# Performance work log

Hardware: AMD Instinct MI355X
Metric: run time of the kernel (lower is better)

Reference implementation:

```python
import math
import jax, jax.numpy as jnp
import numpy as np

B = 8          # number of graphs in the batch
NMAX = 256     # max nodes per graph (padding size)
K = 128        # num_kernels
H = 32         # num_heads
NTYPE = 101    # max_node_type + 1


def setup_inputs() -> dict:
    key = jax.random.key(0)
    ks = jax.random.split(key, 10)
    sizes = np.asarray(NMAX - np.arange(B) * 16, dtype=np.int32)  # 256,240,...,144 -> ragged
    N = int(sizes.sum())  # 1600
    coord = jax.random.normal(ks[0], (N, 3), dtype=jnp.float32) * 3.0
    node_type = jax.random.randint(ks[1], (N,), 0, NTYPE, dtype=jnp.int32)
    gaussian_means = jax.random.uniform(ks[2], (1, K), minval=0.0, maxval=3.0, dtype=jnp.float32)
    gaussian_stds = jax.random.uniform(ks[3], (1, K), minval=0.0, maxval=3.0, dtype=jnp.float32)
    # nn.Embedding(max_node_type+1, 2) tables; original init is const(0)/const(1),
    # we perturb so the computation is non-degenerate.
    mul_w = jax.random.normal(ks[4], (NTYPE, 2), dtype=jnp.float32) * 0.1
    bias_w = 1.0 + jax.random.normal(ks[5], (NTYPE, 2), dtype=jnp.float32) * 0.1
    W1 = jax.random.normal(ks[6], (K, K), dtype=jnp.float32) / math.sqrt(K)
    b1 = jnp.zeros((K,), dtype=jnp.float32)
    W2 = jax.random.normal(ks[7], (K, H), dtype=jnp.float32) / math.sqrt(K)
    b2 = jnp.zeros((H,), dtype=jnp.float32)
    return {
        "coord": coord,
        "gaussian_means": gaussian_means,
        "gaussian_stds": gaussian_stds,
        "mul_w": mul_w,
        "bias_w": bias_w,
        "W1": W1,
        "b1": b1,
        "W2": W2,
        "b2": b2,
        "node_type": node_type,
        "batch_num_nodes": jnp.asarray(sizes),
    }


def reference(coord, gaussian_means, gaussian_stds, mul_w, bias_w, W1, b1, W2, b2,
              node_type, batch_num_nodes):
    N = coord.shape[0]
    offsets = jnp.concatenate([jnp.zeros((1,), dtype=batch_num_nodes.dtype),
                               jnp.cumsum(batch_num_nodes)[:-1]])
    ar = jnp.arange(NMAX)
    idx = offsets[:, None] + ar[None, :]                     # [B, n] flat node index per graph slot
    valid = ar[None, :] < batch_num_nodes[:, None]           # [B, n] node mask
    idx_c = jnp.clip(idx, 0, N - 1)
    pc = coord[idx_c]                                        # [B, n, 3] padded coords
    pt = node_type[idx_c]                                    # [B, n]

    # pairwise Euclidean distance (torch.cdist p=2), sqrt-safe at 0
    diff = pc[:, :, None, :] - pc[:, None, :, :]             # [B, n, n, 3]
    sq = jnp.sum(diff * diff, axis=-1)                       # [B, n, n]
    nz = sq > 0
    dist = jnp.where(nz, jnp.sqrt(jnp.where(nz, sq, 1.0)), 0.0)

    # outer-sum of per-node (src, dst) scaling embeddings
    mul_e = mul_w[pt]                                        # [B, n, 2]
    bias_e = bias_w[pt]
    mul = mul_e[:, :, None, 0] + mul_e[:, None, :, 1]        # [B, n, n]
    bias = bias_e[:, :, None, 0] + bias_e[:, None, :, 1]
    scaled = mul * dist + bias                               # [B, n, n]

    means = gaussian_means.reshape(-1)                       # [K]
    stds = jnp.abs(gaussian_stds.reshape(-1)) + 0.01         # [K]
    z = (scaled[..., None] - means) / stds                   # [B, n, n, K]
    gk = jnp.exp(-0.5 * z * z) / (-math.sqrt(2.0 * math.pi) * stds)

    h = jax.nn.gelu(gk @ W1 + b1, approximate=False)         # exact gelu like torch F.gelu
    out = h @ W2 + b2                                        # [B, n, n, H]

    pair = valid[:, :, None] & valid[:, None, :]             # padded positions -> -inf
    return jnp.where(pair[..., None], out, -jnp.inf)
```

## Files before the change

### kernel.cpp

```cpp
#include <hip/hip_runtime.h>
#include <math.h>

#define NMAXC 256
#define KC 128
#define HC 32
#define BC 8
#define TP 128
#define NEG_SENTINEL (-1.0e30f)
#define LOG2E 1.4426950408889634f

typedef __bf16 bf16x8 __attribute__((ext_vector_type(8)));
typedef float  f32x16 __attribute__((ext_vector_type(16)));
union FragU { uint4 u; bf16x8 v; };

#define EXP2F(x) __builtin_amdgcn_exp2f(x)

__device__ __forceinline__ unsigned pack2(float lo, float hi) {
    return __builtin_amdgcn_perm(__float_as_uint(hi), __float_as_uint(lo), 0x07060302u);
}

__global__ __launch_bounds__(256) void se3d_prep(const float* __restrict__ W1,
                                                 const float* __restrict__ W2,
                                                 const float* __restrict__ gm,
                                                 const float* __restrict__ gs,
                                                 unsigned* __restrict__ wsu) {
    int t = blockIdx.x * 256 + threadIdx.x;
    if (t < 2048) {
        int f = t >> 6, l = t & 63;
        int mt = f >> 3, ks = f & 7;
        int c  = mt * 32 + (l & 31);
        int k0 = ks * 16 + 8 * (l >> 5);
        unsigned u[4];
#pragma unroll
        for (int p = 0; p < 4; ++p)
            u[p] = pack2(-W1[(k0 + 2 * p) * KC + c], -W1[(k0 + 2 * p + 1) * KC + c]);
        ((uint4*)wsu)[t] = make_uint4(u[0], u[1], u[2], u[3]);
    } else if (t < 2560) {
        int x = t - 2048;
        int ft = x >> 6, l = x & 63;
        int hi = l >> 5, ln = l & 31;
        unsigned u[4];
#pragma unroll
        for (int d = 0; d < 4; ++d) {
            int c0 = 32 * (ft >> 1) + 16 * (ft & 1) + 8 * (d >> 1) + 4 * hi + 2 * (d & 1);
            u[d] = pack2(W2[c0 * HC + ln], W2[(c0 + 1) * HC + ln]);
        }
        ((uint4*)wsu)[2048 + x] = make_uint4(u[0], u[1], u[2], u[3]);
    } else if (t < 2688) {
        int k = t - 2560;
        float inv = 1.0f / (fabsf(gs[k]) + 0.01f);
        float m   = gm[k];
        float A2  = -0.5f * inv * inv * LOG2E;
        float* wf = (float*)wsu + 10240;
        wf[k]       = A2;
        wf[128 + k] = -2.0f * A2 * m;
        wf[256 + k] = A2 * m * m + log2f(0.3989422804014327f * inv);
    }
}

__global__ __launch_bounds__(256, 4) void se3d_main(
    const float* __restrict__ coord, const float* __restrict__ mulw,
    const float* __restrict__ biasw, const float* __restrict__ b1,
    const float* __restrict__ b2, const int* __restrict__ ntype,
    const int* __restrict__ bnn, const void* __restrict__ ws,
    float* __restrict__ out)
{
    __shared__ __attribute__((aligned(16))) float cst[544];

    const int b = blockIdx.y;
    const int n = bnn[b];
    const int q0 = blockIdx.x * TP;
    const int tid = threadIdx.x;

    if (q0 >= n * n) {
        int v = q0 + (tid >> 1) - n * n;
        int wdt = 256 - n;
        int na = n * wdt;
        int i, j;
        if (v < na) { i = v / wdt; j = n + (v - i * wdt); }
        else        { int vp = v - na; i = n + (vp >> 8); j = vp & 255; }
        float4 s4 = make_float4(NEG_SENTINEL, NEG_SENTINEL, NEG_SENTINEL, NEG_SENTINEL);
        float4* o = (float4*)(out + ((size_t)((b * NMAXC + i) * NMAXC + j)) * HC)
                  + (tid & 1) * 4;
#pragma unroll
        for (int t = 0; t < 4; ++t) o[t] = s4;
        return;
    }

    if (tid < 136) {
        uint4 v;
        if (tid < 96)       v = ((const uint4*)((const char*)ws + 40960))[tid];
        else if (tid < 128) v = ((const uint4*)b1)[tid - 96];
        else                v = ((const uint4*)b2)[tid - 128];
        ((uint4*)cst)[tid] = v;
    }
    int off = 0;
    for (int t = 0; t < b; ++t) off += bnn[t];
    __syncthreads();

    const int l = tid & 63, w = tid >> 6;
    const int hi = l >> 5, ln = l & 31;

    int q = q0 + w * 32 + ln;
    int i = q / n;
    int j = q - i * n;
    int gi = off + i, gj = off + j;
    float dx = coord[gi * 3 + 0] - coord[gj * 3 + 0];
    float dy = coord[gi * 3 + 1] - coord[gj * 3 + 1];
    float dz = coord[gi * 3 + 2] - coord[gj * 3 + 2];
    float sq = dx * dx + dy * dy + dz * dz;
    float dist = sq > 0.f ? sqrtf(sq) : 0.f;
    int ti = ntype[gi], tj = ntype[gj];
    float s = (mulw[ti * 2 + 0] + mulw[tj * 2 + 1]) * dist
            + (biasw[ti * 2 + 0] + biasw[tj * 2 + 1]);
    size_t obase = ((size_t)((b * NMAXC + i) * NMAXC + j)) * HC;

    const float4*  c4  = (const float4*)cst;
    const bf16x8*  w1t = (const bf16x8*)ws;
    const bf16x8*  w2t = (const bf16x8*)((const char*)ws + 32768);

    FragU gf[8];
#pragma unroll
    for (int ks = 0; ks < 8; ++ks) {
        int b4 = 4 * ks + 2 * hi;
        float4 a0 = c4[b4],      a1 = c4[b4 + 1];
        float4 p0 = c4[32 + b4], p1 = c4[32 + b4 + 1];
        float4 c0 = c4[64 + b4], c1 = c4[64 + b4 + 1];
        float g0 = EXP2F(fmaf(fmaf(a0.x, s, p0.x), s, c0.x));
        float g1 = EXP2F(fmaf(fmaf(a0.y, s, p0.y), s, c0.y));
        float g2 = EXP2F(fmaf(fmaf(a0.z, s, p0.z), s, c0.z));
        float g3 = EXP2F(fmaf(fmaf(a0.w, s, p0.w), s, c0.w));
        float g4 = EXP2F(fmaf(fmaf(a1.x, s, p1.x), s, c1.x));
        float g5 = EXP2F(fmaf(fmaf(a1.y, s, p1.y), s, c1.y));
        float g6 = EXP2F(fmaf(fmaf(a1.z, s, p1.z), s, c1.z));
        float g7 = EXP2F(fmaf(fmaf(a1.w, s, p1.w), s, c1.w));
        gf[ks].u.x = pack2(g0, g1);
        gf[ks].u.y = pack2(g2, g3);
        gf[ks].u.z = pack2(g4, g5);
        gf[ks].u.w = pack2(g6, g7);
    }

    f32x16 c2;
#pragma unroll
    for (int qd = 0; qd < 4; ++qd) {
        float4 bv = c4[128 + 2 * qd + hi];
        c2[4 * qd + 0] = bv.x; c2[4 * qd + 1] = bv.y;
        c2[4 * qd + 2] = bv.z; c2[4 * qd + 3] = bv.w;
    }

    const float KSG = -1.702f * LOG2E;

#pragma unroll
    for (int nt = 0; nt < 4; ++nt) {
        f32x16 acc;
#pragma unroll
        for (int qd = 0; qd < 4; ++qd) {
            float4 bv = c4[96 + 8 * nt + 2 * qd + hi];
            acc[4 * qd + 0] = bv.x; acc[4 * qd + 1] = bv.y;
            acc[4 * qd + 2] = bv.z; acc[4 * qd + 3] = bv.w;
        }
#pragma unroll
        for (int ks = 0; ks < 8; ++ks) {
            bf16x8 af = w1t[(nt * 8 + ks) * 64 + l];
            acc = __builtin_amdgcn_mfma_f32_32x32x16_bf16(af, gf[ks].v, acc, 0, 0, 0);
        }
        unsigned hpk8[8];
#pragma unroll
        for (int g8 = 0; g8 < 8; ++g8) {
            float x0 = acc[2 * g8], x1 = acc[2 * g8 + 1];
            float gl0 = x0 * __builtin_amdgcn_rcpf(1.0f + EXP2F(x0 * KSG));
            float gl1 = x1 * __builtin_amdgcn_rcpf(1.0f + EXP2F(x1 * KSG));
            hpk8[g8] = pack2(gl0, gl1);
        }
        FragU hf0, hf1;
        hf0.u = make_uint4(hpk8[0], hpk8[1], hpk8[2], hpk8[3]);
        hf1.u = make_uint4(hpk8[4], hpk8[5], hpk8[6], hpk8[7]);
        c2 = __builtin_amdgcn_mfma_f32_32x32x16_bf16(w2t[(2 * nt) * 64 + l], hf0.v, c2, 0, 0, 0);
        c2 = __builtin_amdgcn_mfma_f32_32x32x16_bf16(w2t[(2 * nt + 1) * 64 + l], hf1.v, c2, 0, 0, 0);
    }

#pragma unroll
    for (int qd = 0; qd < 4; ++qd) {
        float4 v = make_float4(c2[4 * qd], c2[4 * qd + 1], c2[4 * qd + 2], c2[4 * qd + 3]);
        *(float4*)(out + obase + 8 * qd + 4 * hi) = v;
    }
}

extern "C" void kernel_launch(void* const* d_in, const int* in_sizes, int n_in,
                              void* d_out, int out_size, void* d_ws, size_t ws_size,
                              hipStream_t stream) {
    const float* coord = (const float*)d_in[0];
    const float* gm    = (const float*)d_in[1];
    const float* gs    = (const float*)d_in[2];
    const float* mulw  = (const float*)d_in[3];
    const float* biasw = (const float*)d_in[4];
    const float* W1    = (const float*)d_in[5];
    const float* b1    = (const float*)d_in[6];
    const float* W2    = (const float*)d_in[7];
    const float* b2    = (const float*)d_in[8];
    const int* ntype   = (const int*)d_in[9];
    const int* bnn     = (const int*)d_in[10];
    float* out = (float*)d_out;

    hipLaunchKernelGGL(se3d_prep, dim3(11), dim3(256), 0, stream,
                       W1, W2, gm, gs, (unsigned*)d_ws);
    hipLaunchKernelGGL(se3d_main, dim3(NMAXC * NMAXC / TP, BC), dim3(256),
                       0, stream,
                       coord, mulw, biasw, b1, b2, ntype, bnn, d_ws, out);
}
```

Measured before the change: 126.0 us.

## Stage MLP weights in LDS and process 512 pairs per block in row layout

New measurement: 122.2 us. 3.0% less time.

```diff
diff --git a/kernel.cpp b/kernel.cpp
--- a/kernel.cpp
+++ b/kernel.cpp
@@ -5,7 +5,6 @@
 #define KC 128
 #define HC 32
 #define BC 8
-#define TP 128
 #define NEG_SENTINEL (-1.0e30f)
 #define LOG2E 1.4426950408889634f
 
@@ -58,131 +57,154 @@
     }
 }
 
-__global__ __launch_bounds__(256, 4) void se3d_main(
+__global__ __launch_bounds__(256, 3) void se3d_main(
     const float* __restrict__ coord, const float* __restrict__ mulw,
     const float* __restrict__ biasw, const float* __restrict__ b1,
     const float* __restrict__ b2, const int* __restrict__ ntype,
     const int* __restrict__ bnn, const void* __restrict__ ws,
     float* __restrict__ out)
 {
-    __shared__ __attribute__((aligned(16))) float cst[544];
-
-    const int b = blockIdx.y;
-    const int n = bnn[b];
-    const int q0 = blockIdx.x * TP;
+    __shared__ __attribute__((aligned(16))) uint4 S[2696];
+
+    const int b   = blockIdx.y;
+    const int n   = bnn[b];
+    const int bx  = blockIdx.x;
     const int tid = threadIdx.x;
-
-    if (q0 >= n * n) {
-        int v = q0 + (tid >> 1) - n * n;
-        int wdt = 256 - n;
-        int na = n * wdt;
-        int i, j;
-        if (v < na) { i = v / wdt; j = n + (v - i * wdt); }
-        else        { int vp = v - na; i = n + (vp >> 8); j = vp & 255; }
-        float4 s4 = make_float4(NEG_SENTINEL, NEG_SENTINEL, NEG_SENTINEL, NEG_SENTINEL);
-        float4* o = (float4*)(out + ((size_t)((b * NMAXC + i) * NMAXC + j)) * HC)
-                  + (tid & 1) * 4;
-#pragma unroll
-        for (int t = 0; t < 4; ++t) o[t] = s4;
+    const int blk0 = bx << 9;
+    const size_t outF = ((size_t)b << 16) * HC;
+
+    if ((bx << 1) >= n) {
+        float4 s4v = make_float4(NEG_SENTINEL, NEG_SENTINEL, NEG_SENTINEL, NEG_SENTINEL);
+        float4* o = (float4*)(out + outF + (size_t)blk0 * HC);
+        for (int x = tid; x < 4096; x += 256) o[x] = s4v;
         return;
     }
 
-    if (tid < 136) {
-        uint4 v;
-        if (tid < 96)       v = ((const uint4*)((const char*)ws + 40960))[tid];
-        else if (tid < 128) v = ((const uint4*)b1)[tid - 96];
-        else                v = ((const uint4*)b2)[tid - 128];
-        ((uint4*)cst)[tid] = v;
+    {
+        const uint4* w4 = (const uint4*)ws;
+        for (int x = tid; x < 2656; x += 256) S[x] = w4[x];
+        if (tid < 32) S[2656 + tid] = ((const uint4*)b1)[tid];
+        if (tid < 8)  S[2688 + tid] = ((const uint4*)b2)[tid];
     }
     int off = 0;
     for (int t = 0; t < b; ++t) off += bnn[t];
     __syncthreads();
 
-    const int l = tid & 63, w = tid >> 6;
-    const int hi = l >> 5, ln = l & 31;
-
-    int q = q0 + w * 32 + ln;
-    int i = q / n;
-    int j = q - i * n;
-    int gi = off + i, gj = off + j;
-    float dx = coord[gi * 3 + 0] - coord[gj * 3 + 0];
-    float dy = coord[gi * 3 + 1] - coord[gj * 3 + 1];
-    float dz = coord[gi * 3 + 2] - coord[gj * 3 + 2];
-    float sq = dx * dx + dy * dy + dz * dz;
-    float dist = sq > 0.f ? sqrtf(sq) : 0.f;
-    int ti = ntype[gi], tj = ntype[gj];
-    float s = (mulw[ti * 2 + 0] + mulw[tj * 2 + 1]) * dist
-            + (biasw[ti * 2 + 0] + biasw[tj * 2 + 1]);
-    size_t obase = ((size_t)((b * NMAXC + i) * NMAXC + j)) * HC;
-
-    const float4*  c4  = (const float4*)cst;
-    const bf16x8*  w1t = (const bf16x8*)ws;
-    const bf16x8*  w2t = (const bf16x8*)((const char*)ws + 32768);
-
-    FragU gf[8];
-#pragma unroll
-    for (int ks = 0; ks < 8; ++ks) {
-        int b4 = 4 * ks + 2 * hi;
-        float4 a0 = c4[b4],      a1 = c4[b4 + 1];
-        float4 p0 = c4[32 + b4], p1 = c4[32 + b4 + 1];
-        float4 c0 = c4[64 + b4], c1 = c4[64 + b4 + 1];
-        float g0 = EXP2F(fmaf(fmaf(a0.x, s, p0.x), s, c0.x));
-        float g1 = EXP2F(fmaf(fmaf(a0.y, s, p0.y), s, c0.y));
-        float g2 = EXP2F(fmaf(fmaf(a0.z, s, p0.z), s, c0.z));
-        float g3 = EXP2F(fmaf(fmaf(a0.w, s, p0.w), s, c0.w));
-        float g4 = EXP2F(fmaf(fmaf(a1.x, s, p1.x), s, c1.x));
-        float g5 = EXP2F(fmaf(fmaf(a1.y, s, p1.y), s, c1.y));
-        float g6 = EXP2F(fmaf(fmaf(a1.z, s, p1.z), s, c1.z));
-        float g7 = EXP2F(fmaf(fmaf(a1.w, s, p1.w), s, c1.w));
-        gf[ks].u.x = pack2(g0, g1);
-        gf[ks].u.y = pack2(g2, g3);
-        gf[ks].u.z = pack2(g4, g5);
-        gf[ks].u.w = pack2(g6, g7);
-    }
-
-    f32x16 c2;
-#pragma unroll
-    for (int qd = 0; qd < 4; ++qd) {
-        float4 bv = c4[128 + 2 * qd + hi];
-        c2[4 * qd + 0] = bv.x; c2[4 * qd + 1] = bv.y;
-        c2[4 * qd + 2] = bv.z; c2[4 * qd + 3] = bv.w;
-    }
-
-    const float KSG = -1.702f * LOG2E;
-
-#pragma unroll
-    for (int nt = 0; nt < 4; ++nt) {
-        f32x16 acc;
+    const bf16x8* w1f = (const bf16x8*)S;
+    const bf16x8* w2f = (const bf16x8*)(S + 2048);
+    const float4* c4  = (const float4*)(S + 2560);
+    const float4* b14 = (const float4*)(S + 2656);
+    const float4* b24 = (const float4*)(S + 2688);
+
+    const int l = tid & 63, w = tid >> 6, hi = l >> 5, ln = l & 31;
+    const int tw0 = blk0 + (w << 7);
+    const int i   = tw0 >> 8;
+    const int j0b = tw0 & 255;
+    const int gi  = off + i;
+
+    const float cx = coord[gi * 3 + 0], cy = coord[gi * 3 + 1], cz = coord[gi * 3 + 2];
+    const int   ti = ntype[gi];
+    const float mI = mulw[ti * 2 + 0], bI = biasw[ti * 2 + 0];
+
+    float sv[4];
+    int   jok[4];
+#pragma unroll
+    for (int t2 = 0; t2 < 4; ++t2) {
+        int j  = j0b + (t2 << 5) + ln;
+        jok[t2] = j < n;
+        int jc = j < n ? j : n - 1;
+        int gj = off + jc;
+        float dx = cx - coord[gj * 3 + 0];
+        float dy = cy - coord[gj * 3 + 1];
+        float dz = cz - coord[gj * 3 + 2];
+        float sq = dx * dx + dy * dy + dz * dz;
+        float dist = sq > 0.f ? sqrtf(sq) : 0.f;
+        int tj = ntype[gj];
+        sv[t2] = (mI + mulw[tj * 2 + 1]) * dist + (bI + biasw[tj * 2 + 1]);
+    }
+
+    const float  KSG  = -1.702f * LOG2E;
+    const float4 SEN4 = make_float4(NEG_SENTINEL, NEG_SENTINEL, NEG_SENTINEL, NEG_SENTINEL);
+
+#pragma unroll
+    for (int t2 = 0; t2 < 4; ++t2) {
+        float* op = out + outF + (size_t)(tw0 + (t2 << 5) + ln) * HC + (hi << 2);
+        if (j0b + (t2 << 5) >= n) {
+#pragma unroll
+            for (int qd = 0; qd < 4; ++qd) *(float4*)(op + (qd << 3)) = SEN4;
+            continue;
+        }
+        const float s = sv[t2];
+
+        FragU gf[8];
+#pragma unroll
+        for (int ks = 0; ks < 8; ++ks) {
+            int b4 = 4 * ks + 2 * hi;
+            float4 a0 = c4[b4],      a1 = c4[b4 + 1];
+            float4 p0 = c4[32 + b4], p1 = c4[32 + b4 + 1];
+            float4 q0 = c4[64 + b4], q1 = c4[64 + b4 + 1];
+            float g0 = EXP2F(fmaf(fmaf(a0.x, s, p0.x), s, q0.x));
+            float g1 = EXP2F(fmaf(fmaf(a0.y, s, p0.y), s, q0.y));
+            float g2 = EXP2F(fmaf(fmaf(a0.z, s, p0.z), s, q0.z));
+            float g3 = EXP2F(fmaf(fmaf(a0.w, s, p0.w), s, q0.w));
+            float g4 = EXP2F(fmaf(fmaf(a1.x, s, p1.x), s, q1.x));
+            float g5 = EXP2F(fmaf(fmaf(a1.y, s, p1.y), s, q1.y));
+            float g6 = EXP2F(fmaf(fmaf(a1.z, s, p1.z), s, q1.z));
+            float g7 = EXP2F(fmaf(fmaf(a1.w, s, p1.w), s, q1.w));
+            gf[ks].u.x = pack2(g0, g1);
+            gf[ks].u.y = pack2(g2, g3);
+            gf[ks].u.z = pack2(g4, g5);
+            gf[ks].u.w = pack2(g6, g7);
+        }
+
+        f32x16 c2;
 #pragma unroll
         for (int qd = 0; qd < 4; ++qd) {
-            float4 bv = c4[96 + 8 * nt + 2 * qd + hi];
-            acc[4 * qd + 0] = bv.x; acc[4 * qd + 1] = bv.y;
-            acc[4 * qd + 2] = bv.z; acc[4 * qd + 3] = bv.w;
-        }
-#pragma unroll
-        for (int ks = 0; ks < 8; ++ks) {
-            bf16x8 af = w1t[(nt * 8 + ks) * 64 + l];
-            acc = __builtin_amdgcn_mfma_f32_32x32x16_bf16(af, gf[ks].v, acc, 0, 0, 0);
-        }
-        unsigned hpk8[8];
-#pragma unroll
-        for (int g8 = 0; g8 < 8; ++g8) {
-            float x0 = acc[2 * g8], x1 = acc[2 * g8 + 1];
-            float gl0 = x0 * __builtin_amdgcn_rcpf(1.0f + EXP2F(x0 * KSG));
-            float gl1 = x1 * __builtin_amdgcn_rcpf(1.0f + EXP2F(x1 * KSG));
-            hpk8[g8] = pack2(gl0, gl1);
-        }
-        FragU hf0, hf1;
-        hf0.u = make_uint4(hpk8[0], hpk8[1], hpk8[2], hpk8[3]);
-        hf1.u = make_uint4(hpk8[4], hpk8[5], hpk8[6], hpk8[7]);
-        c2 = __builtin_amdgcn_mfma_f32_32x32x16_bf16(w2t[(2 * nt) * 64 + l], hf0.v, c2, 0, 0, 0);
-        c2 = __builtin_amdgcn_mfma_f32_32x32x16_bf16(w2t[(2 * nt + 1) * 64 + l], hf1.v, c2, 0, 0, 0);
-    }
-
-#pragma unroll
-    for (int qd = 0; qd < 4; ++qd) {
-        float4 v = make_float4(c2[4 * qd], c2[4 * qd + 1], c2[4 * qd + 2], c2[4 * qd + 3]);
-        *(float4*)(out + obase + 8 * qd + 4 * hi) = v;
+            float4 bv = b24[2 * qd + hi];
+            c2[4 * qd + 0] = bv.x; c2[4 * qd + 1] = bv.y;
+            c2[4 * qd + 2] = bv.z; c2[4 * qd + 3] = bv.w;
+        }
+
+#pragma unroll
+        for (int nt = 0; nt < 4; ++nt) {
+            f32x16 acc;
+#pragma unroll
+            for (int qd = 0; qd < 4; ++qd) {
+                float4 bv = b14[8 * nt + 2 * qd + hi];
+                acc[4 * qd + 0] = bv.x; acc[4 * qd + 1] = bv.y;
+                acc[4 * qd + 2] = bv.z; acc[4 * qd + 3] = bv.w;
+            }
+#pragma unroll
+            for (int ks = 0; ks < 8; ++ks)
+                acc = __builtin_amdgcn_mfma_f32_32x32x16_bf16(w1f[(nt * 8 + ks) * 64 + l],
+                                                              gf[ks].v, acc, 0, 0, 0);
+            unsigned hpk8[8];
+#pragma unroll
+            for (int g8 = 0; g8 < 8; ++g8) {
+                float x0 = acc[2 * g8], x1 = acc[2 * g8 + 1];
+                float gl0 = x0 * __builtin_amdgcn_rcpf(1.0f + EXP2F(x0 * KSG));
+                float gl1 = x1 * __builtin_amdgcn_rcpf(1.0f + EXP2F(x1 * KSG));
+                hpk8[g8] = pack2(gl0, gl1);
+            }
+            FragU hf0, hf1;
+            hf0.u = make_uint4(hpk8[0], hpk8[1], hpk8[2], hpk8[3]);
+            hf1.u = make_uint4(hpk8[4], hpk8[5], hpk8[6], hpk8[7]);
+            c2 = __builtin_amdgcn_mfma_f32_32x32x16_bf16(w2f[(2 * nt) * 64 + l],
+                                                         hf0.v, c2, 0, 0, 0);
+            c2 = __builtin_amdgcn_mfma_f32_32x32x16_bf16(w2f[(2 * nt + 1) * 64 + l],
+                                                         hf1.v, c2, 0, 0, 0);
+        }
+
+        const bool v = jok[t2] != 0;
+#pragma unroll
+        for (int qd = 0; qd < 4; ++qd) {
+            float4 vv;
+            vv.x = v ? c2[4 * qd + 0] : NEG_SENTINEL;
+            vv.y = v ? c2[4 * qd + 1] : NEG_SENTINEL;
+            vv.z = v ? c2[4 * qd + 2] : NEG_SENTINEL;
+            vv.w = v ? c2[4 * qd + 3] : NEG_SENTINEL;
+            *(float4*)(op + (qd << 3)) = vv;
+        }
     }
 }
 
@@ -204,7 +226,7 @@
 
     hipLaunchKernelGGL(se3d_prep, dim3(11), dim3(256), 0, stream,
                        W1, W2, gm, gs, (unsigned*)d_ws);
-    hipLaunchKernelGGL(se3d_main, dim3(NMAXC * NMAXC / TP, BC), dim3(256),
+    hipLaunchKernelGGL(se3d_main, dim3(128, BC), dim3(256),
                        0, stream,
                        coord, mulw, biasw, b1, b2, ntype, bnn, d_ws, out);
 }
```
